# Optimization experiments

Hardware: AMD Instinct MI355X
Metric: run time of the kernel (lower is better)

Reference implementation:

```python
import jax, jax.numpy as jnp
import numpy as np

B, S, H, E, K = 4, 2048, 1024, 8, 2


def setup_inputs() -> dict:
    key = jax.random.key(0)
    k0, k1, k2 = jax.random.split(key, 3)
    x = jax.random.normal(k0, (B, S, H), dtype=jnp.float32)
    # gate: Linear(H -> E); torch stores W as [out,in], we keep [E,H]
    gate_w = jax.random.normal(k1, (E, H), dtype=jnp.float32) * 0.02
    gate_b = jnp.zeros((E,), dtype=jnp.float32)
    # experts: E x Linear(H -> H); stored as [E, H_in, H_out]
    expert_w = jax.random.normal(k2, (E, H, H), dtype=jnp.float32) * 0.02
    expert_b = jnp.zeros((E, H), dtype=jnp.float32)
    return {"x": x, "gate_w": gate_w, "gate_b": gate_b,
            "expert_w": expert_w, "expert_b": expert_b}


def reference(x, gate_w, gate_b, expert_w, expert_b):
    bsz, seq_len, h = x.shape
    xt = x.reshape(-1, h)                      # [T, H]
    T = xt.shape[0]

    # router (moe_router): softmax -> top-k -> renormalize
    logits = xt @ gate_w.T + gate_b            # [T, E]
    routing_probs = jax.nn.softmax(logits, axis=-1)
    top_k_probs, top_k_index = jax.lax.top_k(routing_probs, K)
    top_k_probs = top_k_probs / jnp.sum(top_k_probs, axis=1, keepdims=True)
    top_k_probs = top_k_probs.astype(x.dtype)

    # combine weights: scatter normalized top-k probs into [T, E]
    rows = jnp.arange(T)[:, None]
    combine = jnp.zeros((T, E), dtype=x.dtype).at[rows, top_k_index].add(top_k_probs)

    # per-expert FFN over all tokens, then weighted combine
    # (equivalent math to the gather / index_add loop: zero weights contribute zero)
    y = jnp.einsum('th,eho->teo', xt, expert_w) + expert_b[None, :, :]  # [T, E, H]
    out = jnp.einsum('te,teh->th', combine, y)                          # [T, H]

    final_output = out.reshape(bsz, seq_len, h)
    return final_output, top_k_index, routing_probs
```

## Files before the change

kernel.cpp:

```cpp
#include <hip/hip_runtime.h>
#include <hip/hip_bf16.h>
#include <stdint.h>

typedef unsigned short ushort_t;
typedef __bf16 bf16x8 __attribute__((ext_vector_type(8)));
typedef float f32x4 __attribute__((ext_vector_type(4)));

#define T_TOK 8192
#define H_DIM 1024
#define E_EXP 8
#define BM 128
#define BN 128
#define BK 64
#define NKT (H_DIM / BK)
#define NWG_G 2304

#define CNT_STRIDE 64
#define RTOK 32
#define RBLOCKS (T_TOK / RTOK)
#define TP_BLOCKS ((H_DIM / 32) * (H_DIM / 32) * E_EXP)

static __device__ __forceinline__ ushort_t f2bf(float f) {
  union { float f; uint32_t u; } c; c.f = f;
  uint32_t u = c.u;
  uint32_t r = u + 0x7FFFu + ((u >> 16) & 1u);
  return (ushort_t)(r >> 16);
}

__global__ __launch_bounds__(256) void router_transpose(
    const float* __restrict__ x, const float* __restrict__ gw,
    const float* __restrict__ gb, const float* __restrict__ ew,
    float* __restrict__ out_idx, float* __restrict__ out_probs,
    int* __restrict__ counts, int* __restrict__ tok, float* __restrict__ wts,
    ushort_t* __restrict__ x_bf, ushort_t* __restrict__ wT)
{
  __shared__ int   sm_eid[RTOK * 2];
  __shared__ float sm_wt[RTOK * 2];
  __shared__ int   lcnt[E_EXP], lbase[E_EXP], lpos[E_EXP];
  __shared__ float tile[32][33];

  const int tid = threadIdx.x;

  if (blockIdx.x >= RBLOCKS) {
    const int tb = blockIdx.x - RBLOCKS;
    const int e = tb >> 10;
    const int n0 = (tb & 31) * 32, k0 = ((tb >> 5) & 31) * 32;
    const float* we = ew + (size_t)e * H_DIM * H_DIM;
    ushort_t* wTe = wT + (size_t)e * H_DIM * H_DIM;
    const int tx = tid & 31, ty = tid >> 5;
#pragma unroll
    for (int i = 0; i < 4; i++)
      tile[ty + 8 * i][tx] = we[(size_t)(k0 + ty + 8 * i) * H_DIM + n0 + tx];
    __syncthreads();
#pragma unroll
    for (int i = 0; i < 4; i++)
      wTe[(size_t)(n0 + ty + 8 * i) * H_DIM + k0 + tx] = f2bf(tile[tx][ty + 8 * i]);
    return;
  }

  const int wave = tid >> 6, l = tid & 63;
  if (tid < E_EXP) { lcnt[tid] = 0; lpos[tid] = 0; }
  __syncthreads();

  const int t0 = blockIdx.x * RTOK;
  for (int it = 0; it < RTOK / 4; it++) {
    const int lt = wave * (RTOK / 4) + it;
    const int t = t0 + lt;
    const float* xt = x + (size_t)t * H_DIM;
    float acc[E_EXP];
#pragma unroll
    for (int e = 0; e < E_EXP; e++) acc[e] = 0.f;
#pragma unroll
    for (int i = 0; i < 4; i++) {
      const int h = (i * 64 + l) * 4;
      const float4 xv = *reinterpret_cast<const float4*>(xt + h);
      ushort4 b;
      b.x = f2bf(xv.x); b.y = f2bf(xv.y); b.z = f2bf(xv.z); b.w = f2bf(xv.w);
      *reinterpret_cast<ushort4*>(x_bf + (size_t)t * H_DIM + h) = b;
#pragma unroll
      for (int e = 0; e < E_EXP; e++) {
        const float4 g = *reinterpret_cast<const float4*>(gw + e * H_DIM + h);
        acc[e] += xv.x * g.x + xv.y * g.y + xv.z * g.z + xv.w * g.w;
      }
    }
#pragma unroll
    for (int e = 0; e < E_EXP; e++) {
      float v = acc[e];
#pragma unroll
      for (int off = 32; off; off >>= 1) v += __shfl_xor(v, off);
      acc[e] = v;
    }
    if (l == 0) {
      float lg[E_EXP], pb[E_EXP];
      float m = -1e30f;
#pragma unroll
      for (int e = 0; e < E_EXP; e++) { lg[e] = acc[e] + gb[e]; m = fmaxf(m, lg[e]); }
      float s = 0.f;
#pragma unroll
      for (int e = 0; e < E_EXP; e++) { pb[e] = expf(lg[e] - m); s += pb[e]; }
      const float inv = 1.f / s;
#pragma unroll
      for (int e = 0; e < E_EXP; e++) {
        pb[e] *= inv;
        out_probs[(size_t)t * E_EXP + e] = pb[e];
      }
      int i0 = 0; float p0 = pb[0];
#pragma unroll
      for (int e = 1; e < E_EXP; e++) if (pb[e] > p0) { p0 = pb[e]; i0 = e; }
      int i1 = -1; float p1 = -1.f;
#pragma unroll
      for (int e = 0; e < E_EXP; e++) if (e != i0 && pb[e] > p1) { p1 = pb[e]; i1 = e; }
      out_idx[(size_t)t * 2 + 0] = (float)i0;
      out_idx[(size_t)t * 2 + 1] = (float)i1;
      const float rn = 1.f / (p0 + p1);
      sm_eid[lt * 2 + 0] = i0; sm_wt[lt * 2 + 0] = p0 * rn;
      sm_eid[lt * 2 + 1] = i1; sm_wt[lt * 2 + 1] = p1 * rn;
    }
  }
  __syncthreads();

  if (tid < RTOK * 2) atomicAdd(&lcnt[sm_eid[tid]], 1);
  __syncthreads();
  if (tid < E_EXP) lbase[tid] = atomicAdd(&counts[tid * CNT_STRIDE], lcnt[tid]);
  __syncthreads();
  if (tid < RTOK * 2) {
    const int e = sm_eid[tid];
    const int p = lbase[e] + atomicAdd(&lpos[e], 1);
    const int dst = e * T_TOK + p;
    tok[dst] = (t0 + (tid >> 1)) * 2 + (tid & 1);
    wts[dst] = sm_wt[tid];
  }
}

#define GLDS16(gp, lp)                                                         \
  __builtin_amdgcn_global_load_lds(                                            \
      (const __attribute__((address_space(1))) void*)(gp),                     \
      (__attribute__((address_space(3))) void*)(lp), 16, 0, 0)

__global__ __launch_bounds__(256, 4) void moe_gemm(
    const ushort_t* __restrict__ x_bf, const ushort_t* __restrict__ wT,
    const float* __restrict__ bias, int* __restrict__ counts,
    const int* __restrict__ tok, const float* __restrict__ wts,
    ushort_t* __restrict__ y)
{
  __shared__ __align__(16) ushort_t As[2 * 4096];
  __shared__ __align__(16) ushort_t Bs[2 * 4096];
  __shared__ int stok[BM];
  __shared__ float swt[BM];
  __shared__ int s_spill;

  const int tid = threadIdx.x;
  const int bid = blockIdx.x;

  int ne[E_EXP], fl[E_EXP];
#pragma unroll
  for (int i = 0; i < E_EXP; i++) {
    ne[i] = counts[i * CNT_STRIDE];
    fl[i] = ne[i] >> 7;
  }

  const int l = tid & 63;
  const int wid = tid >> 6;
  const int fr = l & 15;
  const int g = l >> 4;

  if (bid < 2048) {
    int e = bid & 7;
    int q = bid >> 3;
    const int home = fl[e] * 8;
    if (q >= (home < 256 ? home : 256)) {
      int sc[E_EXP], spill_total = 0;
#pragma unroll
      for (int i = 0; i < E_EXP; i++) {
        sc[i] = fl[i] * 8 > 256 ? fl[i] * 8 - 256 : 0;
        spill_total += sc[i];
      }
      if (spill_total == 0) return;
      if (tid == 0) s_spill = atomicAdd(&counts[520], 1);
      __syncthreads();
      int k = s_spill;
      if (k >= spill_total) return;
      int done = 0;
#pragma unroll
      for (int i = 0; i < E_EXP; i++) {
        if (!done) { if (k < sc[i]) { e = i; done = 1; } else k -= sc[i]; }
      }
      q = 256 + k;
    }
    const int mt = q >> 3;
    const int nt = q & 7;

    if (tid < BM) {
      stok[tid] = tok[e * T_TOK + mt * BM + tid];
      swt[tid] = wts[e * T_TOK + mt * BM + tid];
    }
    __syncthreads();

    const int r0 = tid >> 2;
    const int cp = (tid & 3) ^ ((tid >> 3) & 3);
    const ushort_t* wTe = wT + (size_t)e * H_DIM * H_DIM;
    const ushort_t* aP0 = x_bf + (size_t)(stok[r0] >> 1) * H_DIM + cp * 8;
    const ushort_t* aP1 = x_bf + (size_t)(stok[r0 + 64] >> 1) * H_DIM + cp * 8;
    const ushort_t* bP0 = wTe + (size_t)(nt * BN + r0) * H_DIM + cp * 8;
    const ushort_t* bP1 = wTe + (size_t)(nt * BN + r0 + 64) * H_DIM + cp * 8;
    const int d0 = tid * 8;
    const int d1 = (tid + 256) * 8;

#define STAGE8(t)                                                              \
  do {                                                                         \
    GLDS16(aP0 + (t) * BK +  0, &As[0 * 4096 + d0]);                           \
    GLDS16(aP1 + (t) * BK +  0, &As[0 * 4096 + d1]);                           \
    GLDS16(aP0 + (t) * BK + 32, &As[1 * 4096 + d0]);                           \
    GLDS16(aP1 + (t) * BK + 32, &As[1 * 4096 + d1]);                           \
    GLDS16(bP0 + (t) * BK +  0, &Bs[0 * 4096 + d0]);                           \
    GLDS16(bP1 + (t) * BK +  0, &Bs[0 * 4096 + d1]);                           \
    GLDS16(bP0 + (t) * BK + 32, &Bs[1 * 4096 + d0]);                           \
    GLDS16(bP1 + (t) * BK + 32, &Bs[1 * 4096 + d1]);                           \
  } while (0)

    const int wm = wid >> 1, wn = wid & 1;
    const int sl = g ^ ((l >> 1) & 3);
    const int arow0 = wm * 64 + fr;
    const int brow0 = wn * 64 + fr;

    f32x4 acc[4][4] = {};

#pragma unroll 1
    for (int t = 0; t < NKT; ++t) {
      if (t) __syncthreads();
      STAGE8(t);
      __syncthreads();
#pragma unroll
      for (int kk = 0; kk < 2; kk++) {
        bf16x8 af[4], bv[4];
#pragma unroll
        for (int mi = 0; mi < 4; mi++)
          af[mi] = *reinterpret_cast<const bf16x8*>(
              &As[kk * 4096 + (arow0 + mi * 16) * 32 + sl * 8]);
#pragma unroll
        for (int nj = 0; nj < 4; nj++)
          bv[nj] = *reinterpret_cast<const bf16x8*>(
              &Bs[kk * 4096 + (brow0 + nj * 16) * 32 + sl * 8]);
        __builtin_amdgcn_s_setprio(1);
#pragma unroll
        for (int mi = 0; mi < 4; mi++)
#pragma unroll
          for (int nj = 0; nj < 4; nj++)
            acc[mi][nj] = __builtin_amdgcn_mfma_f32_16x16x32_bf16(
                af[mi], bv[nj], acc[mi][nj], 0, 0, 0);
        __builtin_amdgcn_s_setprio(0);
      }
    }

    float bias4[4];
#pragma unroll
    for (int nj = 0; nj < 4; nj++)
      bias4[nj] = bias[e * H_DIM + nt * BN + wn * 64 + nj * 16 + fr];
#pragma unroll
    for (int mi = 0; mi < 4; mi++) {
      const int rr0 = wm * 64 + mi * 16 + g * 4;
#pragma unroll
      for (int r = 0; r < 4; r++) {
        const int row = rr0 + r;
        const float wgt = swt[row];
        ushort_t* yr = y + (size_t)stok[row] * H_DIM;
#pragma unroll
        for (int nj = 0; nj < 4; nj++) {
          const int n = nt * BN + wn * 64 + nj * 16 + fr;
          yr[n] = f2bf(wgt * (acc[mi][nj][r] + bias4[nj]));
        }
      }
    }
  } else {
    const int e = bid & 7;
    const int tq = (bid - 2048) >> 3;
    const int rem = ne[e] - (fl[e] << 7);
    const int tcnt = (rem + 63) >> 6;
    if (tq >= tcnt * 8) return;
    const int mtt = tq >> 3;
    const int ntt = tq & 7;
    const int row0 = (fl[e] << 7) + mtt * 64;
    int valid = ne[e] - row0; if (valid > 64) valid = 64;

    if (tid < 64) {
      int slot = row0 + tid;
      if (slot >= ne[e]) slot = ne[e] - 1;
      stok[tid] = tok[e * T_TOK + slot];
      swt[tid] = wts[e * T_TOK + slot];
    }
    __syncthreads();

    const ushort_t* wTe = wT + (size_t)e * H_DIM * H_DIM;
    const int trow = tid >> 3;
    const int tlc = (tid & 7) ^ (trow & 7);
    const ushort_t* taS0 = x_bf + (size_t)(stok[trow] >> 1) * H_DIM + tlc * 8;
    const ushort_t* taS1 = x_bf + (size_t)(stok[trow + 32] >> 1) * H_DIM + tlc * 8;
    const ushort_t* tbS0 = wTe + (size_t)(ntt * 128 + trow) * H_DIM + tlc * 8;
    const ushort_t* tbS1 = tbS0 + (size_t)32 * H_DIM;
    const ushort_t* tbS2 = tbS0 + (size_t)64 * H_DIM;
    const ushort_t* tbS3 = tbS0 + (size_t)96 * H_DIM;

#define TSTAGE1(t)                                                             \
  do {                                                                         \
    GLDS16(taS0 + (t) * BK, &As[tid * 8]);                                     \
    GLDS16(taS1 + (t) * BK, &As[(tid + 256) * 8]);                             \
    GLDS16(tbS0 + (t) * BK, &Bs[tid * 8]);                                     \
    GLDS16(tbS1 + (t) * BK, &Bs[(tid + 256) * 8]);                             \
    GLDS16(tbS2 + (t) * BK, &Bs[(tid + 512) * 8]);                             \
    GLDS16(tbS3 + (t) * BK, &Bs[(tid + 768) * 8]);                             \
  } while (0)

    const int tph0 = (g ^ (fr & 7)) * 8;
    const int tph1 = ((4 ^ g) ^ (fr & 7)) * 8;

    f32x4 tacc[2][4] = {};

#pragma unroll 1
    for (int t = 0; t < NKT; ++t) {
      if (t) __syncthreads();
      TSTAGE1(t);
      __syncthreads();
#pragma unroll
      for (int kk = 0; kk < 2; kk++) {
        const int ph = kk ? tph1 : tph0;
#pragma unroll
        for (int nf = 0; nf < 2; nf++) {
          const bf16x8 tbv = *reinterpret_cast<const bf16x8*>(
              &Bs[(wid * 32 + nf * 16 + fr) * 64 + ph]);
#pragma unroll
          for (int mi = 0; mi < 4; mi++) {
            const bf16x8 tav = *reinterpret_cast<const bf16x8*>(
                &As[(mi * 16 + fr) * 64 + ph]);
            tacc[nf][mi] = __builtin_amdgcn_mfma_f32_16x16x32_bf16(
                tav, tbv, tacc[nf][mi], 0, 0, 0);
          }
        }
      }
    }

#pragma unroll
    for (int nf = 0; nf < 2; nf++) {
      const int ncol = ntt * 128 + wid * 32 + nf * 16 + fr;
      const float bs = bias[e * H_DIM + ncol];
#pragma unroll
      for (int mi = 0; mi < 4; mi++) {
        const int rb = mi * 16 + g * 4;
#pragma unroll
        for (int r = 0; r < 4; r++) {
          const int row = rb + r;
          if (row < valid) {
            ushort_t* yr = y + (size_t)stok[row] * H_DIM;
            yr[ncol] = f2bf(swt[row] * (tacc[nf][mi][r] + bs));
          }
        }
      }
    }
  }
}

__global__ __launch_bounds__(256) void combine_kernel(
    const ushort_t* __restrict__ y, float* __restrict__ out)
{
  const int t = blockIdx.x;
  const ushort_t* r0 = y + (size_t)(t * 2) * H_DIM;
  const ushort_t* r1 = r0 + H_DIM;
  float* o = out + (size_t)t * H_DIM;
  const int h = threadIdx.x * 4;
  const ushort4 u0 = *reinterpret_cast<const ushort4*>(r0 + h);
  const ushort4 u1 = *reinterpret_cast<const ushort4*>(r1 + h);
  float4 v;
  union { uint32_t u; float f; } c;
  c.u = (uint32_t)u0.x << 16; v.x = c.f; c.u = (uint32_t)u1.x << 16; v.x += c.f;
  c.u = (uint32_t)u0.y << 16; v.y = c.f; c.u = (uint32_t)u1.y << 16; v.y += c.f;
  c.u = (uint32_t)u0.z << 16; v.z = c.f; c.u = (uint32_t)u1.z << 16; v.z += c.f;
  c.u = (uint32_t)u0.w << 16; v.w = c.f; c.u = (uint32_t)u1.w << 16; v.w += c.f;
  *reinterpret_cast<float4*>(o + h) = v;
}

extern "C" void kernel_launch(void* const* d_in, const int* in_sizes, int n_in,
                              void* d_out, int out_size, void* d_ws, size_t ws_size,
                              hipStream_t stream)
{
  const float* x  = (const float*)d_in[0];
  const float* gw = (const float*)d_in[1];
  const float* gb = (const float*)d_in[2];
  const float* ew = (const float*)d_in[3];
  const float* eb = (const float*)d_in[4];

  float* out = (float*)d_out;
  float* out_final = out;
  float* out_idx   = out + (size_t)T_TOK * H_DIM;
  float* out_probs = out_idx + (size_t)T_TOK * 2;

  char* ws = (char*)d_ws;
  size_t off = 0;
  int*      counts  = (int*)(ws + off); off += 4096;
  int*      tok     = (int*)(ws + off); off += (size_t)E_EXP * T_TOK * 4;
  float*    wts     = (float*)(ws + off); off += (size_t)E_EXP * T_TOK * 4;
  ushort_t* x_bf    = (ushort_t*)(ws + off); off += (size_t)T_TOK * H_DIM * 2;
  ushort_t* wT      = (ushort_t*)(ws + off); off += (size_t)E_EXP * H_DIM * H_DIM * 2;
  ushort_t* y       = (ushort_t*)(ws + off); off += (size_t)T_TOK * 2 * H_DIM * 2;

  hipMemsetAsync(counts, 0, 4096, stream);

  router_transpose<<<RBLOCKS + TP_BLOCKS, 256, 0, stream>>>(
      x, gw, gb, ew, out_idx, out_probs, counts, tok, wts, x_bf, wT);
  moe_gemm<<<NWG_G, 256, 0, stream>>>(x_bf, wT, eb, counts, tok, wts, y);
  combine_kernel<<<T_TOK, 256, 0, stream>>>(y, out_final);
}
```

Measured before the change: 93.84 us.

## Fuse top-k combine into GEMM epilogue via float atomics into zeroed output

Removes the combine kernel and the bf16 intermediate y buffer. The router kernel now zeroes the final fp32 output, and the GEMM epilogue atomically adds each weighted expert result directly into it. This saves a launch and a full write and read of the intermediate, but introduces scattered uncoalesced fp32 atomics, with two per output element. The GEMM launch bound also drops from 4 to 3 waves per SIMD, which may reduce occupancy in exchange for more registers.

```diff
diff --git a/kernel.cpp b/kernel.cpp
--- a/kernel.cpp
+++ b/kernel.cpp
@@ -30,6 +30,7 @@
 __global__ __launch_bounds__(256) void router_transpose(
     const float* __restrict__ x, const float* __restrict__ gw,
     const float* __restrict__ gb, const float* __restrict__ ew,
+    float* __restrict__ out_final,
     float* __restrict__ out_idx, float* __restrict__ out_probs,
     int* __restrict__ counts, int* __restrict__ tok, float* __restrict__ wts,
     ushort_t* __restrict__ x_bf, ushort_t* __restrict__ wT)
@@ -60,9 +61,18 @@
 
   const int wave = tid >> 6, l = tid & 63;
   if (tid < E_EXP) { lcnt[tid] = 0; lpos[tid] = 0; }
+
+  const int t0 = blockIdx.x * RTOK;
+
+  {
+    float4 z4 = make_float4(0.f, 0.f, 0.f, 0.f);
+    float4* oz = reinterpret_cast<float4*>(out_final + (size_t)t0 * H_DIM);
+#pragma unroll
+    for (int i = 0; i < (RTOK * H_DIM / 4) / 256; i++)
+      oz[tid + i * 256] = z4;
+  }
   __syncthreads();
 
-  const int t0 = blockIdx.x * RTOK;
   for (int it = 0; it < RTOK / 4; it++) {
     const int lt = wave * (RTOK / 4) + it;
     const int t = t0 + lt;
@@ -127,7 +137,7 @@
     const int e = sm_eid[tid];
     const int p = lbase[e] + atomicAdd(&lpos[e], 1);
     const int dst = e * T_TOK + p;
-    tok[dst] = (t0 + (tid >> 1)) * 2 + (tid & 1);
+    tok[dst] = t0 + (tid >> 1);
     wts[dst] = sm_wt[tid];
   }
 }
@@ -137,11 +147,11 @@
       (const __attribute__((address_space(1))) void*)(gp),                     \
       (__attribute__((address_space(3))) void*)(lp), 16, 0, 0)
 
-__global__ __launch_bounds__(256, 4) void moe_gemm(
+__global__ __launch_bounds__(256, 3) void moe_gemm(
     const ushort_t* __restrict__ x_bf, const ushort_t* __restrict__ wT,
     const float* __restrict__ bias, int* __restrict__ counts,
     const int* __restrict__ tok, const float* __restrict__ wts,
-    ushort_t* __restrict__ y)
+    float* __restrict__ out)
 {
   __shared__ __align__(16) ushort_t As[2 * 4096];
   __shared__ __align__(16) ushort_t Bs[2 * 4096];
@@ -199,8 +209,8 @@
     const int r0 = tid >> 2;
     const int cp = (tid & 3) ^ ((tid >> 3) & 3);
     const ushort_t* wTe = wT + (size_t)e * H_DIM * H_DIM;
-    const ushort_t* aP0 = x_bf + (size_t)(stok[r0] >> 1) * H_DIM + cp * 8;
-    const ushort_t* aP1 = x_bf + (size_t)(stok[r0 + 64] >> 1) * H_DIM + cp * 8;
+    const ushort_t* aP0 = x_bf + (size_t)stok[r0] * H_DIM + cp * 8;
+    const ushort_t* aP1 = x_bf + (size_t)stok[r0 + 64] * H_DIM + cp * 8;
     const ushort_t* bP0 = wTe + (size_t)(nt * BN + r0) * H_DIM + cp * 8;
     const ushort_t* bP1 = wTe + (size_t)(nt * BN + r0 + 64) * H_DIM + cp * 8;
     const int d0 = tid * 8;
@@ -263,11 +273,11 @@
       for (int r = 0; r < 4; r++) {
         const int row = rr0 + r;
         const float wgt = swt[row];
-        ushort_t* yr = y + (size_t)stok[row] * H_DIM;
+        float* orow = out + (size_t)stok[row] * H_DIM;
 #pragma unroll
         for (int nj = 0; nj < 4; nj++) {
           const int n = nt * BN + wn * 64 + nj * 16 + fr;
-          yr[n] = f2bf(wgt * (acc[mi][nj][r] + bias4[nj]));
+          atomicAdd(&orow[n], wgt * (acc[mi][nj][r] + bias4[nj]));
         }
       }
     }
@@ -293,8 +303,8 @@
     const ushort_t* wTe = wT + (size_t)e * H_DIM * H_DIM;
     const int trow = tid >> 3;
     const int tlc = (tid & 7) ^ (trow & 7);
-    const ushort_t* taS0 = x_bf + (size_t)(stok[trow] >> 1) * H_DIM + tlc * 8;
-    const ushort_t* taS1 = x_bf + (size_t)(stok[trow + 32] >> 1) * H_DIM + tlc * 8;
+    const ushort_t* taS0 = x_bf + (size_t)stok[trow] * H_DIM + tlc * 8;
+    const ushort_t* taS1 = x_bf + (size_t)stok[trow + 32] * H_DIM + tlc * 8;
     const ushort_t* tbS0 = wTe + (size_t)(ntt * 128 + trow) * H_DIM + tlc * 8;
     const ushort_t* tbS1 = tbS0 + (size_t)32 * H_DIM;
     const ushort_t* tbS2 = tbS0 + (size_t)64 * H_DIM;
@@ -349,32 +359,13 @@
         for (int r = 0; r < 4; r++) {
           const int row = rb + r;
           if (row < valid) {
-            ushort_t* yr = y + (size_t)stok[row] * H_DIM;
-            yr[ncol] = f2bf(swt[row] * (tacc[nf][mi][r] + bs));
+            float* orow = out + (size_t)stok[row] * H_DIM;
+            atomicAdd(&orow[ncol], swt[row] * (tacc[nf][mi][r] + bs));
           }
         }
       }
     }
   }
-}
-
-__global__ __launch_bounds__(256) void combine_kernel(
-    const ushort_t* __restrict__ y, float* __restrict__ out)
-{
-  const int t = blockIdx.x;
-  const ushort_t* r0 = y + (size_t)(t * 2) * H_DIM;
-  const ushort_t* r1 = r0 + H_DIM;
-  float* o = out + (size_t)t * H_DIM;
-  const int h = threadIdx.x * 4;
-  const ushort4 u0 = *reinterpret_cast<const ushort4*>(r0 + h);
-  const ushort4 u1 = *reinterpret_cast<const ushort4*>(r1 + h);
-  float4 v;
-  union { uint32_t u; float f; } c;
-  c.u = (uint32_t)u0.x << 16; v.x = c.f; c.u = (uint32_t)u1.x << 16; v.x += c.f;
-  c.u = (uint32_t)u0.y << 16; v.y = c.f; c.u = (uint32_t)u1.y << 16; v.y += c.f;
-  c.u = (uint32_t)u0.z << 16; v.z = c.f; c.u = (uint32_t)u1.z << 16; v.z += c.f;
-  c.u = (uint32_t)u0.w << 16; v.w = c.f; c.u = (uint32_t)u1.w << 16; v.w += c.f;
-  *reinterpret_cast<float4*>(o + h) = v;
 }
 
 extern "C" void kernel_launch(void* const* d_in, const int* in_sizes, int n_in,
@@ -399,12 +390,10 @@
   float*    wts     = (float*)(ws + off); off += (size_t)E_EXP * T_TOK * 4;
   ushort_t* x_bf    = (ushort_t*)(ws + off); off += (size_t)T_TOK * H_DIM * 2;
   ushort_t* wT      = (ushort_t*)(ws + off); off += (size_t)E_EXP * H_DIM * H_DIM * 2;
-  ushort_t* y       = (ushort_t*)(ws + off); off += (size_t)T_TOK * 2 * H_DIM * 2;
 
   hipMemsetAsync(counts, 0, 4096, stream);
 
   router_transpose<<<RBLOCKS + TP_BLOCKS, 256, 0, stream>>>(
-      x, gw, gb, ew, out_idx, out_probs, counts, tok, wts, x_bf, wT);
-  moe_gemm<<<NWG_G, 256, 0, stream>>>(x_bf, wT, eb, counts, tok, wts, y);
-  combine_kernel<<<T_TOK, 256, 0, stream>>>(y, out_final);
+      x, gw, gb, ew, out_final, out_idx, out_probs, counts, tok, wts, x_bf, wT);
+  moe_gemm<<<NWG_G, 256, 0, stream>>>(x_bf, wT, eb, counts, tok, wts, out_final);
 }
```

Result: slower. 124.5 us (+32.7%).
